# Kernel tuning notes

Hardware: AMD Instinct MI355X
Metric: run time of the kernel (lower is better)

Reference implementation:

```python
import jax, jax.numpy as jnp
import numpy as np

LATENT_DIM = 64
K = 128


def setup_inputs() -> dict:
    key = jax.random.key(0)
    ks = jax.random.split(key, 7)
    B, T, N, d, k = 64, 1024, 1024, LATENT_DIM, K
    return {
        "review_seq": jax.random.normal(ks[0], (B, T, d), dtype=jnp.float32),
        "post_seq": jax.random.normal(ks[1], (B, N, d), dtype=jnp.float32),
        "Wl": jax.random.normal(ks[2], (d, d), dtype=jnp.float32) * 0.05,
        "Wr": jax.random.normal(ks[3], (k, d), dtype=jnp.float32) * 0.05,
        "Wp": jax.random.normal(ks[4], (k, d), dtype=jnp.float32) * 0.05,
        "whr": jax.random.normal(ks[5], (1, k), dtype=jnp.float32) * 0.05,
        "whp": jax.random.normal(ks[6], (1, k), dtype=jnp.float32) * 0.05,
    }


def reference(review_seq, post_seq, Wl, Wr, Wp, whr, whp):
    # L[b,t,n] = tanh(review @ Wl @ post^T)
    L = jnp.tanh(jnp.einsum('btd,dD,bnD->btn', review_seq, Wl, post_seq))
    # Hp[b,k,n] = tanh(Wp @ post^T + Wr @ review^T @ L)
    Hp = jnp.tanh(jnp.einsum('kd,bnd->bkn', Wp, post_seq)
                  + jnp.einsum('kd,btd,btn->bkn', Wr, review_seq, L))
    # Hr[b,k,t] = tanh(Wr @ review^T + Wp @ post^T @ L^T)
    Hr = jnp.tanh(jnp.einsum('kd,btd->bkt', Wr, review_seq)
                  + jnp.einsum('kd,bnd,btn->bkt', Wp, post_seq, L))
    # attention weights over post (n) and review (t) positions
    Ap = jax.nn.softmax(jnp.einsum('yk,bkn->bn', whp, Hp), axis=-1)
    Ar = jax.nn.softmax(jnp.einsum('yk,bkt->bt', whr, Hr), axis=-1)
    co_p = jnp.einsum('bnd,bn->bd', post_seq, Ap)
    co_r = jnp.einsum('btd,bt->bd', review_seq, Ar)
    return jnp.concatenate([co_p, co_r], axis=1)  # [B, 2*latent_dim]
```

## Files before the change

### kernel.cpp

```cpp
#include <hip/hip_runtime.h>
#include <hip/hip_bf16.h>


typedef __attribute__((ext_vector_type(8))) short bfrag;
typedef __attribute__((ext_vector_type(4))) float ffrag;

typedef const __attribute__((address_space(1))) unsigned GAS_U;
typedef __attribute__((address_space(3))) unsigned LAS_U;

__device__ __forceinline__ void gload16(const void* g, void* l) {
  __builtin_amdgcn_global_load_lds((GAS_U*)g, (LAS_U*)l, 16, 0, 0);
}

__device__ __forceinline__ unsigned short f2b(float f) {
  unsigned u = __builtin_bit_cast(unsigned, f);
  u += 0x7FFFu + ((u >> 16) & 1u);
  return (unsigned short)(u >> 16);
}
__device__ __forceinline__ float b2f(unsigned short h) {
  return __builtin_bit_cast(float, (unsigned)h << 16);
}
__device__ __forceinline__ float ftanh(float x) {
  float e = __builtin_amdgcn_exp2f(x * 2.88539008177792681f);
  return fmaf(-2.0f, __builtin_amdgcn_rcpf(e + 1.0f), 1.0f);
}
__device__ __forceinline__ unsigned cvtpk(float lo, float hi) {
  unsigned r;
  asm("v_cvt_pk_bf16_f32 %0, %1, %2" : "=v"(r) : "v"(lo), "v"(hi));
  return r;
}

#define MFMA(a, b, c) __builtin_amdgcn_mfma_f32_16x16x32_bf16((a), (b), (c), 0, 0, 0)

__global__ __launch_bounds__(256) void prep_kernel(
    const float* __restrict__ review, const float* __restrict__ post,
    const float* __restrict__ Wl, const float* __restrict__ Wr,
    const float* __restrict__ Wp,
    unsigned short* __restrict__ RWb, unsigned short* __restrict__ Rb,
    unsigned short* __restrict__ Pb, unsigned short* __restrict__ postb)
{
  const int chunk = blockIdx.x, b = blockIdx.y, side = blockIdx.z;
  const int tid = threadIdx.x, lane = tid & 63, w = tid >> 6;
  const int lr = lane & 15, lg = lane >> 4;
  const int r0 = chunk * 128;

  __shared__ __align__(16) unsigned short seqs[128][72];
  __shared__ __align__(16) unsigned short wgt[128][72];
  __shared__ __align__(16) unsigned short wlt[64][72];

  const float* seq = (side == 0) ? review : post;
#pragma unroll
  for (int jj = 0; jj < 8; ++jj) {
    int e = tid + jj * 256;
    int r = e >> 4, d4 = (e & 15) * 4;
    float4 v = *(const float4*)(seq + ((size_t)(b * 1024 + r0 + r)) * 64 + d4);
    unsigned lo = ((unsigned)f2b(v.y) << 16) | f2b(v.x);
    unsigned hi = ((unsigned)f2b(v.w) << 16) | f2b(v.z);
    *(uint2*)&seqs[r][d4] = make_uint2(lo, hi);
    if (side == 1)
      *(uint2*)(postb + ((size_t)(b * 1024 + r0 + r)) * 64 + d4) = make_uint2(lo, hi);
  }
  const float* wkd = (side == 0) ? Wr : Wp;
#pragma unroll
  for (int jj = 0; jj < 8; ++jj) {
    int e = tid + jj * 256;
    int k = e >> 4, d4 = (e & 15) * 4;
    float4 v = *(const float4*)(wkd + k * 64 + d4);
    unsigned lo = ((unsigned)f2b(v.y) << 16) | f2b(v.x);
    unsigned hi = ((unsigned)f2b(v.w) << 16) | f2b(v.z);
    *(uint2*)&wgt[k][d4] = make_uint2(lo, hi);
  }
  if (side == 0) {
    for (int i = tid; i < 64 * 64; i += 256) {
      int d = i >> 6, c = i & 63;
      wlt[c][d] = f2b(Wl[d * 64 + c]);
    }
  }
  __syncthreads();

  if (side == 0) {
    ffrag acc[2][4] = {};
#pragma unroll
    for (int ks = 0; ks < 2; ++ks)
#pragma unroll
      for (int ts = 0; ts < 2; ++ts) {
        bfrag a = *(const bfrag*)&seqs[w * 32 + ts * 16 + lr][ks * 32 + lg * 8];
#pragma unroll
        for (int is = 0; is < 4; ++is) {
          bfrag bb = *(const bfrag*)&wlt[is * 16 + lr][ks * 32 + lg * 8];
          acc[ts][is] = MFMA(a, bb, acc[ts][is]);
        }
      }
#pragma unroll
    for (int ts = 0; ts < 2; ++ts)
#pragma unroll
      for (int is = 0; is < 4; ++is)
#pragma unroll
        for (int j = 0; j < 4; ++j) {
          int t = r0 + w * 32 + ts * 16 + lg * 4 + j;
          int i2 = is * 16 + lr;
          RWb[((size_t)(b * 1024 + t)) * 64 + i2] = f2b(acc[ts][is][j]);
        }
  }
  {
    ffrag acc[2][8] = {};
#pragma unroll
    for (int ks = 0; ks < 2; ++ks)
#pragma unroll
      for (int ksb = 0; ksb < 2; ++ksb) {
        bfrag a = *(const bfrag*)&wgt[w * 32 + ksb * 16 + lr][ks * 32 + lg * 8];
#pragma unroll
        for (int ts = 0; ts < 8; ++ts) {
          bfrag bb = *(const bfrag*)&seqs[ts * 16 + lr][ks * 32 + lg * 8];
          acc[ksb][ts] = MFMA(a, bb, acc[ksb][ts]);
        }
      }
    unsigned short* dst = (side == 0) ? Rb : Pb;
#pragma unroll
    for (int ksb = 0; ksb < 2; ++ksb)
#pragma unroll
      for (int ts = 0; ts < 8; ++ts)
#pragma unroll
        for (int j = 0; j < 4; ++j) {
          int k = w * 32 + ksb * 16 + lg * 4 + j;
          int t = r0 + ts * 16 + lr;
          dst[((size_t)(b * 128 + k)) * 1024 + t] = f2b(acc[ksb][ts][j]);
        }
  }
}

__global__ __launch_bounds__(256, 4) void hz_kernel(
    const unsigned short* __restrict__ RWb, const unsigned short* __restrict__ Rb,
    const unsigned short* __restrict__ Pb, const unsigned short* __restrict__ postb,
    const float* __restrict__ whp, const float* __restrict__ whr,
    float* __restrict__ zp, float* __restrict__ zr)
{
  const int orig = blockIdx.x;
  const int swz = (orig & 7) * 128 + (orig >> 3);
  const int strip = swz & 7, pair = swz >> 3;
  const int b = pair & 63, role = pair >> 6;
  const int s0 = strip * 128;
  const int tid = threadIdx.x, lane = tid & 63, w = tid >> 6;
  const int lr = lane & 15, lg = lane >> 4;

  const unsigned short* resident = role ? RWb : postb;
  const unsigned short* chunkseq = role ? postb : RWb;
  const unsigned short* coeff    = role ? Pb : Rb;
  const unsigned short* addterm  = role ? Rb : Pb;
  const float* wh                = role ? whr : whp;
  float* zout                    = role ? zr : zp;

  __shared__ __align__(16) char smem[32768];
  float* zacc = (float*)(smem + 24576);

  const int crow = (w << 3) + (lane >> 3), cslot = lane & 7;
  const char* csrc = (const char*)chunkseq + (size_t)b * 131072
                     + crow * 128 + ((cslot ^ (crow & 7)) << 4);
  const int kk = ((w & 1) << 6) + lane;
  const char* ksrc = (const char*)coeff + (size_t)b * 262144
                     + (size_t)kk * 2048 + (w >> 1) * 16;
  const int woff = w << 10;

  bfrag bb[2][2];
  {
    const char* rbase = (const char*)resident + ((size_t)(b * 1024 + s0)) * 128;
#pragma unroll
    for (int ks = 0; ks < 2; ++ks)
#pragma unroll
      for (int ns = 0; ns < 2; ++ns)
        bb[ks][ns] = *(const bfrag*)(rbase + (w * 32 + ns * 16 + lr) * 128 + ks * 64 + lg * 16);
  }

  gload16(csrc, smem + woff);
  gload16(ksrc, smem + 8192 + woff);
  gload16(ksrc + 32, smem + 12288 + woff);
  __syncthreads();

  ffrag acc[2][8] = {};
  int cur = 0;

#pragma unroll 2
  for (int tc = 0; tc < 32; ++tc) {
    if (tc < 31) {
      const int nb = cur ^ 1;
      const char* cs = csrc + (size_t)(tc + 1) * 4096;
      const char* ks2 = ksrc + (tc + 1) * 64;
      gload16(cs, smem + nb * 4096 + woff);
      gload16(ks2, smem + 8192 + nb * 8192 + woff);
      gload16(ks2 + 32, smem + 8192 + nb * 8192 + 4096 + woff);
    }

    {
      const char* rwc = smem + cur * 4096;
#pragma unroll
      for (int ts = 0; ts < 2; ++ts) {
        ffrag la[2] = {};
#pragma unroll
        for (int ks = 0; ks < 2; ++ks) {
          const int arow = ts * 16 + lr;
          bfrag a = *(const bfrag*)(rwc + arow * 128 + (((ks * 4 + lg) ^ (arow & 7)) << 4));
#pragma unroll
          for (int ns = 0; ns < 2; ++ns)
            la[ns] = MFMA(a, bb[ks][ns], la[ns]);
        }
#pragma unroll
        for (int ns = 0; ns < 2; ++ns) {
          const int res = w * 32 + ns * 16 + lr;
          uint2 pkv;
          pkv.x = cvtpk(ftanh(la[ns][0]), ftanh(la[ns][1]));
          pkv.y = cvtpk(ftanh(la[ns][2]), ftanh(la[ns][3]));
          *(uint2*)(smem + 24576 + (ts * 2 + (lg >> 1)) * 2048 + res * 16 + (lg & 1) * 8) = pkv;
        }
      }
    }
    __syncthreads();

    {
      const char* rlc = smem + 8192 + cur * 8192;
      bfrag a0 = *(const bfrag*)(rlc + lg * 2048 + (w * 32 + lr) * 16);
      bfrag a1 = *(const bfrag*)(rlc + lg * 2048 + (w * 32 + 16 + lr) * 16);
#pragma unroll
      for (int ns = 0; ns < 8; ++ns) {
        bfrag bbr = *(const bfrag*)(smem + 24576 + lg * 2048 + (ns * 16 + lr) * 16);
        acc[0][ns] = MFMA(a0, bbr, acc[0][ns]);
        acc[1][ns] = MFMA(a1, bbr, acc[1][ns]);
      }
    }
    __syncthreads();
    cur ^= 1;
  }

  float zpart[8] = {0, 0, 0, 0, 0, 0, 0, 0};
#pragma unroll
  for (int ksb = 0; ksb < 2; ++ksb)
#pragma unroll
    for (int j = 0; j < 4; ++j) {
      const int k = w * 32 + ksb * 16 + lg * 4 + j;
      const float whk = wh[k];
      const unsigned short* arow = addterm + ((size_t)(b * 128 + k)) * 1024 + s0;
#pragma unroll
      for (int ns = 0; ns < 8; ++ns) {
        const int res = ns * 16 + lr;
        float h = ftanh(acc[ksb][ns][j] + b2f(arow[res]));
        zpart[ns] += whk * h;
      }
    }
#pragma unroll
  for (int ns = 0; ns < 8; ++ns) {
    zpart[ns] += __shfl_xor(zpart[ns], 16);
    zpart[ns] += __shfl_xor(zpart[ns], 32);
  }
  if (lg == 0) {
#pragma unroll
    for (int ns = 0; ns < 8; ++ns) zacc[w * 128 + ns * 16 + lr] = zpart[ns];
  }
  __syncthreads();
  if (tid < 128)
    zout[(size_t)b * 1024 + s0 + tid] =
        zacc[tid] + zacc[128 + tid] + zacc[256 + tid] + zacc[384 + tid];
}

__global__ __launch_bounds__(1024) void final_kernel(
    const float* __restrict__ review, const float* __restrict__ post,
    const float* __restrict__ zp, const float* __restrict__ zr,
    float* __restrict__ out)
{
  const int b = blockIdx.x, side = blockIdx.y, tid = threadIdx.x;
  const int wid = tid >> 6, lane = tid & 63;
  __shared__ float zl[1024];
  __shared__ float red[16];
  __shared__ float cacc[16][64];

  const float* z = (side == 0) ? zp : zr;
  const float* seq = (side == 0) ? post : review;

  float v = z[(size_t)b * 1024 + tid];
  zl[tid] = v;
  float m = v;
#pragma unroll
  for (int off = 32; off; off >>= 1) m = fmaxf(m, __shfl_xor(m, off));
  if (lane == 0) red[wid] = m;
  __syncthreads();
  m = red[0];
#pragma unroll
  for (int i = 1; i < 16; ++i) m = fmaxf(m, red[i]);
  __syncthreads();

  float e = __expf(v - m);
  zl[tid] = e;
  float sm = e;
#pragma unroll
  for (int off = 32; off; off >>= 1) sm += __shfl_xor(sm, off);
  if (lane == 0) red[wid] = sm;
  __syncthreads();
  sm = red[0];
#pragma unroll
  for (int i = 1; i < 16; ++i) sm += red[i];
  const float inv = 1.0f / sm;

  const int d = lane;
  float a = 0.f;
  for (int n = wid * 64; n < wid * 64 + 64; ++n)
    a += zl[n] * seq[((size_t)(b * 1024 + n)) * 64 + d];
  cacc[wid][d] = a;
  __syncthreads();
  if (tid < 64) {
    float s = 0.f;
#pragma unroll
    for (int g = 0; g < 16; ++g) s += cacc[g][tid];
    out[b * 128 + side * 64 + tid] = s * inv;
  }
}

extern "C" void kernel_launch(void* const* d_in, const int* in_sizes, int n_in,
                              void* d_out, int out_size, void* d_ws, size_t ws_size,
                              hipStream_t stream) {
  const float* review = (const float*)d_in[0];
  const float* post   = (const float*)d_in[1];
  const float* Wl     = (const float*)d_in[2];
  const float* Wr     = (const float*)d_in[3];
  const float* Wp     = (const float*)d_in[4];
  const float* whr    = (const float*)d_in[5];
  const float* whp    = (const float*)d_in[6];
  float* out = (float*)d_out;

  char* ws = (char*)d_ws;
  unsigned short* RWb   = (unsigned short*)(ws);
  unsigned short* Rb    = (unsigned short*)(ws + (size_t)8  * 1048576);
  unsigned short* Pb    = (unsigned short*)(ws + (size_t)24 * 1048576);
  unsigned short* postb = (unsigned short*)(ws + (size_t)40 * 1048576);
  float* zp = (float*)(ws + (size_t)48 * 1048576);
  float* zr = (float*)(ws + (size_t)48 * 1048576 + 262144);

  prep_kernel<<<dim3(8, 64, 2), dim3(256), 0, stream>>>(
      review, post, Wl, Wr, Wp, RWb, Rb, Pb, postb);
  hz_kernel<<<dim3(1024), dim3(256), 0, stream>>>(
      RWb, Rb, Pb, postb, whp, whr, zp, zr);
  final_kernel<<<dim3(64, 2), dim3(1024), 0, stream>>>(
      review, post, zp, zr, out);
}
```

Before: 103.7 us.

## Keep tanh(L) tile in registers as MFMA operand, retile coefficient layout

The second GEMM in hz_kernel now takes the tanh'd L tile straight from registers. It feeds the packed bf16 values as operands to a 16x16x16 MFMA instead of writing them to shared memory and reading them back. That removes the LDS round trip and one __syncthreads per iteration. To support this, prep_kernel writes Rb/Pb in a tiled layout that matches the new fragment loads, and the epilogue reduces with lane shuffles instead of through shared memory. The cost is using the smaller-K MFMA instruction (more instructions per FLOP) and an inline-asm accumulator constraint.

```diff
diff --git a/kernel.cpp b/kernel.cpp
--- a/kernel.cpp
+++ b/kernel.cpp
@@ -3,6 +3,7 @@
 
 
 typedef __attribute__((ext_vector_type(8))) short bfrag;
+typedef __attribute__((ext_vector_type(4))) short bfrag4;
 typedef __attribute__((ext_vector_type(4))) float ffrag;
 
 typedef const __attribute__((address_space(1))) unsigned GAS_U;
@@ -31,6 +32,11 @@
 }
 
 #define MFMA(a, b, c) __builtin_amdgcn_mfma_f32_16x16x32_bf16((a), (b), (c), 0, 0, 0)
+
+__device__ __forceinline__ void mfma16(bfrag4 a, bfrag4 b, ffrag& c) {
+  asm volatile("v_mfma_f32_16x16x16_bf16 %0, %1, %2, %0" : "+a"(c) : "v"(a), "v"(b));
+}
+
 
 __global__ __launch_bounds__(256) void prep_kernel(
     const float* __restrict__ review, const float* __restrict__ post,
@@ -115,17 +121,18 @@
           acc[ksb][ts] = MFMA(a, bb, acc[ksb][ts]);
         }
       }
-    unsigned short* dst = (side == 0) ? Rb : Pb;
+    char* dstb = (char*)((side == 0) ? Rb : Pb) + (size_t)b * 262144
+                 + (size_t)chunk * 4 * 8192;
 #pragma unroll
     for (int ksb = 0; ksb < 2; ++ksb)
 #pragma unroll
-      for (int ts = 0; ts < 8; ++ts)
-#pragma unroll
-        for (int j = 0; j < 4; ++j) {
-          int k = w * 32 + ksb * 16 + lg * 4 + j;
-          int t = r0 + ts * 16 + lr;
-          dst[((size_t)(b * 128 + k)) * 1024 + t] = f2b(acc[ksb][ts][j]);
-        }
+      for (int ts2 = 0; ts2 < 8; ++ts2) {
+        char* base = dstb + (ts2 >> 1) * 8192 + (ts2 & 1) * 4096
+                     + (w * 2 + ksb) * 512 + (lr >> 2) * 128 + (lr & 3) * 2;
+#pragma unroll
+        for (int j = 0; j < 4; ++j)
+          *(unsigned short*)(base + (lg * 4 + j) * 8) = f2b(acc[ksb][ts2][j]);
+      }
   }
 }
 
@@ -150,16 +157,13 @@
   const float* wh                = role ? whr : whp;
   float* zout                    = role ? zr : zp;
 
-  __shared__ __align__(16) char smem[32768];
-  float* zacc = (float*)(smem + 24576);
-
-  const int crow = (w << 3) + (lane >> 3), cslot = lane & 7;
+  __shared__ __align__(16) char smem[24576];
+  const int woff = w << 10;
+
+  const int crow = tid >> 3, cslot = tid & 7;
   const char* csrc = (const char*)chunkseq + (size_t)b * 131072
                      + crow * 128 + ((cslot ^ (crow & 7)) << 4);
-  const int kk = ((w & 1) << 6) + lane;
-  const char* ksrc = (const char*)coeff + (size_t)b * 262144
-                     + (size_t)kk * 2048 + (w >> 1) * 16;
-  const int woff = w << 10;
+  const char* ksrc = (const char*)coeff + (size_t)b * 262144 + tid * 16;
 
   bfrag bb[2][2];
   {
@@ -167,97 +171,89 @@
 #pragma unroll
     for (int ks = 0; ks < 2; ++ks)
 #pragma unroll
-      for (int ns = 0; ns < 2; ++ns)
-        bb[ks][ns] = *(const bfrag*)(rbase + (w * 32 + ns * 16 + lr) * 128 + ks * 64 + lg * 16);
+      for (int rs = 0; rs < 2; ++rs)
+        bb[ks][rs] = *(const bfrag*)(rbase + (w * 32 + rs * 16 + lr) * 128 + ks * 64 + lg * 16);
   }
 
   gload16(csrc, smem + woff);
   gload16(ksrc, smem + 8192 + woff);
-  gload16(ksrc + 32, smem + 12288 + woff);
+  gload16(ksrc + 4096, smem + 8192 + 4096 + woff);
   __syncthreads();
 
   ffrag acc[2][8] = {};
-  int cur = 0;
 
 #pragma unroll 2
   for (int tc = 0; tc < 32; ++tc) {
+    const int cur = tc & 1;
     if (tc < 31) {
       const int nb = cur ^ 1;
-      const char* cs = csrc + (size_t)(tc + 1) * 4096;
-      const char* ks2 = ksrc + (tc + 1) * 64;
-      gload16(cs, smem + nb * 4096 + woff);
-      gload16(ks2, smem + 8192 + nb * 8192 + woff);
-      gload16(ks2 + 32, smem + 8192 + nb * 8192 + 4096 + woff);
-    }
-
-    {
-      const char* rwc = smem + cur * 4096;
+      gload16(csrc + (size_t)(tc + 1) * 4096, smem + nb * 4096 + woff);
+      gload16(ksrc + (size_t)(tc + 1) * 8192, smem + 8192 + nb * 8192 + woff);
+      gload16(ksrc + (size_t)(tc + 1) * 8192 + 4096, smem + 8192 + nb * 8192 + 4096 + woff);
+    }
+
+    const char* rwc = smem + cur * 4096;
+    uint2 pk[2][2];
+#pragma unroll
+    for (int ts = 0; ts < 2; ++ts) {
+      ffrag la[2] = {};
+#pragma unroll
+      for (int ks = 0; ks < 2; ++ks) {
+        const int arow = ts * 16 + lr;
+        bfrag a = *(const bfrag*)(rwc + arow * 128 + (((ks * 4 + lg) ^ (arow & 7)) << 4));
+        la[0] = MFMA(a, bb[ks][0], la[0]);
+        la[1] = MFMA(a, bb[ks][1], la[1]);
+      }
+#pragma unroll
+      for (int rs = 0; rs < 2; ++rs) {
+        pk[ts][rs].x = cvtpk(ftanh(la[rs][0]), ftanh(la[rs][1]));
+        pk[ts][rs].y = cvtpk(ftanh(la[rs][2]), ftanh(la[rs][3]));
+      }
+    }
+
+    const char* rlc = smem + 8192 + cur * 8192;
+#pragma unroll
+    for (int kt = 0; kt < 8; ++kt) {
 #pragma unroll
       for (int ts = 0; ts < 2; ++ts) {
-        ffrag la[2] = {};
-#pragma unroll
-        for (int ks = 0; ks < 2; ++ks) {
-          const int arow = ts * 16 + lr;
-          bfrag a = *(const bfrag*)(rwc + arow * 128 + (((ks * 4 + lg) ^ (arow & 7)) << 4));
-#pragma unroll
-          for (int ns = 0; ns < 2; ++ns)
-            la[ns] = MFMA(a, bb[ks][ns], la[ns]);
-        }
-#pragma unroll
-        for (int ns = 0; ns < 2; ++ns) {
-          const int res = w * 32 + ns * 16 + lr;
-          uint2 pkv;
-          pkv.x = cvtpk(ftanh(la[ns][0]), ftanh(la[ns][1]));
-          pkv.y = cvtpk(ftanh(la[ns][2]), ftanh(la[ns][3]));
-          *(uint2*)(smem + 24576 + (ts * 2 + (lg >> 1)) * 2048 + res * 16 + (lg & 1) * 8) = pkv;
-        }
+        bfrag4 bk = *(const bfrag4*)(rlc + ts * 4096 + kt * 512 + lg * 128 + lr * 8);
+        mfma16(__builtin_bit_cast(bfrag4, pk[ts][0]), bk, acc[0][kt]);
+        mfma16(__builtin_bit_cast(bfrag4, pk[ts][1]), bk, acc[1][kt]);
       }
     }
     __syncthreads();
-
-    {
-      const char* rlc = smem + 8192 + cur * 8192;
-      bfrag a0 = *(const bfrag*)(rlc + lg * 2048 + (w * 32 + lr) * 16);
-      bfrag a1 = *(const bfrag*)(rlc + lg * 2048 + (w * 32 + 16 + lr) * 16);
-#pragma unroll
-      for (int ns = 0; ns < 8; ++ns) {
-        bfrag bbr = *(const bfrag*)(smem + 24576 + lg * 2048 + (ns * 16 + lr) * 16);
-        acc[0][ns] = MFMA(a0, bbr, acc[0][ns]);
-        acc[1][ns] = MFMA(a1, bbr, acc[1][ns]);
-      }
-    }
-    __syncthreads();
-    cur ^= 1;
-  }
-
-  float zpart[8] = {0, 0, 0, 0, 0, 0, 0, 0};
-#pragma unroll
-  for (int ksb = 0; ksb < 2; ++ksb)
+  }
+
+  float whs[8];
+#pragma unroll
+  for (int kt = 0; kt < 8; ++kt) whs[kt] = wh[kt * 16 + lr];
+
+  const char* abase = (const char*)addterm + (size_t)b * 262144
+                      + (size_t)(strip * 4 + w) * 8192 + lg * 128 + lr * 8;
+  float zsum[2][4] = {};
+#pragma unroll
+  for (int rs = 0; rs < 2; ++rs)
+#pragma unroll
+    for (int kt = 0; kt < 8; ++kt) {
+      uint2 av = *(const uint2*)(abase + rs * 4096 + kt * 512);
+      const float whk = whs[kt];
+      zsum[rs][0] += whk * ftanh(acc[rs][kt][0] + b2f((unsigned short)(av.x & 0xFFFF)));
+      zsum[rs][1] += whk * ftanh(acc[rs][kt][1] + b2f((unsigned short)(av.x >> 16)));
+      zsum[rs][2] += whk * ftanh(acc[rs][kt][2] + b2f((unsigned short)(av.y & 0xFFFF)));
+      zsum[rs][3] += whk * ftanh(acc[rs][kt][3] + b2f((unsigned short)(av.y >> 16)));
+    }
+#pragma unroll
+  for (int rs = 0; rs < 2; ++rs)
 #pragma unroll
     for (int j = 0; j < 4; ++j) {
-      const int k = w * 32 + ksb * 16 + lg * 4 + j;
-      const float whk = wh[k];
-      const unsigned short* arow = addterm + ((size_t)(b * 128 + k)) * 1024 + s0;
-#pragma unroll
-      for (int ns = 0; ns < 8; ++ns) {
-        const int res = ns * 16 + lr;
-        float h = ftanh(acc[ksb][ns][j] + b2f(arow[res]));
-        zpart[ns] += whk * h;
-      }
-    }
-#pragma unroll
-  for (int ns = 0; ns < 8; ++ns) {
-    zpart[ns] += __shfl_xor(zpart[ns], 16);
-    zpart[ns] += __shfl_xor(zpart[ns], 32);
-  }
-  if (lg == 0) {
-#pragma unroll
-    for (int ns = 0; ns < 8; ++ns) zacc[w * 128 + ns * 16 + lr] = zpart[ns];
-  }
-  __syncthreads();
-  if (tid < 128)
-    zout[(size_t)b * 1024 + s0 + tid] =
-        zacc[tid] + zacc[128 + tid] + zacc[256 + tid] + zacc[384 + tid];
+      float v = zsum[rs][j];
+      v += __shfl_xor(v, 1);
+      v += __shfl_xor(v, 2);
+      v += __shfl_xor(v, 4);
+      v += __shfl_xor(v, 8);
+      if (lr == 0)
+        zout[(size_t)b * 1024 + s0 + w * 32 + rs * 16 + lg * 4 + j] = v;
+    }
 }
 
 __global__ __launch_bounds__(1024) void final_kernel(
```

Result: slower. 184.7 us (+78.0%).

## Split hz_kernel into 64-wide strips with 8 waves per block

Applied to the files above, without the earlier changes.

The hz kernel now handles 64 resident positions per block instead of 128 and runs 8 waves of 512 threads, with a grid of 2048 blocks. Each wave computes one 16x16 L tile and a 16x64 slice of the second GEMM, so per-thread accumulator registers drop from 32 to 16 floats. Only half the waves load the chunk sequence, and the loop is no longer unrolled. The aim is higher occupancy and more parallelism, at the cost of reloading the streamed chunk and coefficient data twice as often overall and doing more cross-wave reduction.

```diff
diff --git a/kernel.cpp b/kernel.cpp
--- a/kernel.cpp
+++ b/kernel.cpp
@@ -129,17 +129,17 @@
   }
 }
 
-__global__ __launch_bounds__(256, 4) void hz_kernel(
+__global__ __launch_bounds__(512, 6) void hz_kernel(
     const unsigned short* __restrict__ RWb, const unsigned short* __restrict__ Rb,
     const unsigned short* __restrict__ Pb, const unsigned short* __restrict__ postb,
     const float* __restrict__ whp, const float* __restrict__ whr,
     float* __restrict__ zp, float* __restrict__ zr)
 {
   const int orig = blockIdx.x;
-  const int swz = (orig & 7) * 128 + (orig >> 3);
-  const int strip = swz & 7, pair = swz >> 3;
+  const int swz = (orig & 7) * 256 + (orig >> 3);
+  const int strip = swz & 15, pair = swz >> 4;
   const int b = pair & 63, role = pair >> 6;
-  const int s0 = strip * 128;
+  const int s0 = strip * 64;
   const int tid = threadIdx.x, lane = tid & 63, w = tid >> 6;
   const int lr = lane & 15, lg = lane >> 4;
 
@@ -150,7 +150,8 @@
   const float* wh                = role ? whr : whp;
   float* zout                    = role ? zr : zp;
 
-  __shared__ __align__(16) char smem[32768];
+  __shared__ __align__(16) char smem[28672];
+  char* ll = smem + 24576;
   float* zacc = (float*)(smem + 24576);
 
   const int crow = (w << 3) + (lane >> 3), cslot = lane & 7;
@@ -161,103 +162,86 @@
                      + (size_t)kk * 2048 + (w >> 1) * 16;
   const int woff = w << 10;
 
-  bfrag bb[2][2];
+  const int ts = w >> 2, rs = w & 3;
+  bfrag rb[2];
   {
     const char* rbase = (const char*)resident + ((size_t)(b * 1024 + s0)) * 128;
 #pragma unroll
     for (int ks = 0; ks < 2; ++ks)
-#pragma unroll
-      for (int ns = 0; ns < 2; ++ns)
-        bb[ks][ns] = *(const bfrag*)(rbase + (w * 32 + ns * 16 + lr) * 128 + ks * 64 + lg * 16);
-  }
-
-  gload16(csrc, smem + woff);
+      rb[ks] = *(const bfrag*)(rbase + (rs * 16 + lr) * 128 + ks * 64 + lg * 16);
+  }
+
+  if (w < 4) gload16(csrc, smem + woff);
   gload16(ksrc, smem + 8192 + woff);
-  gload16(ksrc + 32, smem + 12288 + woff);
-  __syncthreads();
-
-  ffrag acc[2][8] = {};
-  int cur = 0;
-
-#pragma unroll 2
+  __syncthreads();
+
+  ffrag acc[4] = {};
+
+#pragma unroll 1
   for (int tc = 0; tc < 32; ++tc) {
+    const int cur = tc & 1, nb = cur ^ 1;
     if (tc < 31) {
-      const int nb = cur ^ 1;
-      const char* cs = csrc + (size_t)(tc + 1) * 4096;
-      const char* ks2 = ksrc + (tc + 1) * 64;
-      gload16(cs, smem + nb * 4096 + woff);
-      gload16(ks2, smem + 8192 + nb * 8192 + woff);
-      gload16(ks2 + 32, smem + 8192 + nb * 8192 + 4096 + woff);
+      if (w < 4) gload16(csrc + (size_t)(tc + 1) * 4096, smem + nb * 4096 + woff);
+      gload16(ksrc + (size_t)(tc + 1) * 64, smem + 8192 + nb * 8192 + woff);
     }
 
     {
       const char* rwc = smem + cur * 4096;
-#pragma unroll
-      for (int ts = 0; ts < 2; ++ts) {
-        ffrag la[2] = {};
-#pragma unroll
-        for (int ks = 0; ks < 2; ++ks) {
-          const int arow = ts * 16 + lr;
-          bfrag a = *(const bfrag*)(rwc + arow * 128 + (((ks * 4 + lg) ^ (arow & 7)) << 4));
-#pragma unroll
-          for (int ns = 0; ns < 2; ++ns)
-            la[ns] = MFMA(a, bb[ks][ns], la[ns]);
-        }
-#pragma unroll
-        for (int ns = 0; ns < 2; ++ns) {
-          const int res = w * 32 + ns * 16 + lr;
-          uint2 pkv;
-          pkv.x = cvtpk(ftanh(la[ns][0]), ftanh(la[ns][1]));
-          pkv.y = cvtpk(ftanh(la[ns][2]), ftanh(la[ns][3]));
-          *(uint2*)(smem + 24576 + (ts * 2 + (lg >> 1)) * 2048 + res * 16 + (lg & 1) * 8) = pkv;
-        }
+      const int arow = ts * 16 + lr;
+      ffrag la = {};
+#pragma unroll
+      for (int ks = 0; ks < 2; ++ks) {
+        bfrag a = *(const bfrag*)(rwc + arow * 128 + (((ks * 4 + lg) ^ (arow & 7)) << 4));
+        la = MFMA(a, rb[ks], la);
       }
+      uint2 pk;
+      pk.x = cvtpk(ftanh(la[0]), ftanh(la[1]));
+      pk.y = cvtpk(ftanh(la[2]), ftanh(la[3]));
+      *(uint2*)(ll + (ts * 2 + (lg >> 1)) * 1024 + (rs * 16 + lr) * 16 + (lg & 1) * 8) = pk;
     }
     __syncthreads();
 
     {
       const char* rlc = smem + 8192 + cur * 8192;
-      bfrag a0 = *(const bfrag*)(rlc + lg * 2048 + (w * 32 + lr) * 16);
-      bfrag a1 = *(const bfrag*)(rlc + lg * 2048 + (w * 32 + 16 + lr) * 16);
-#pragma unroll
-      for (int ns = 0; ns < 8; ++ns) {
-        bfrag bbr = *(const bfrag*)(smem + 24576 + lg * 2048 + (ns * 16 + lr) * 16);
-        acc[0][ns] = MFMA(a0, bbr, acc[0][ns]);
-        acc[1][ns] = MFMA(a1, bbr, acc[1][ns]);
+      bfrag a0 = *(const bfrag*)(rlc + lg * 2048 + (w * 16 + lr) * 16);
+#pragma unroll
+      for (int nt = 0; nt < 4; ++nt) {
+        bfrag bbr = *(const bfrag*)(ll + lg * 1024 + (nt * 16 + lr) * 16);
+        acc[nt] = MFMA(a0, bbr, acc[nt]);
       }
     }
     __syncthreads();
-    cur ^= 1;
-  }
-
-  float zpart[8] = {0, 0, 0, 0, 0, 0, 0, 0};
-#pragma unroll
-  for (int ksb = 0; ksb < 2; ++ksb)
-#pragma unroll
-    for (int j = 0; j < 4; ++j) {
-      const int k = w * 32 + ksb * 16 + lg * 4 + j;
-      const float whk = wh[k];
-      const unsigned short* arow = addterm + ((size_t)(b * 128 + k)) * 1024 + s0;
-#pragma unroll
-      for (int ns = 0; ns < 8; ++ns) {
-        const int res = ns * 16 + lr;
-        float h = ftanh(acc[ksb][ns][j] + b2f(arow[res]));
-        zpart[ns] += whk * h;
-      }
-    }
-#pragma unroll
-  for (int ns = 0; ns < 8; ++ns) {
-    zpart[ns] += __shfl_xor(zpart[ns], 16);
-    zpart[ns] += __shfl_xor(zpart[ns], 32);
+  }
+
+  const float4 whs4 = *(const float4*)(wh + w * 16 + lg * 4);
+  float zpart[4] = {0, 0, 0, 0};
+#pragma unroll
+  for (int j = 0; j < 4; ++j) {
+    const int k = w * 16 + lg * 4 + j;
+    const float whk = ((const float*)&whs4)[j];
+    const unsigned short* arow = addterm + ((size_t)(b * 128 + k)) * 1024 + s0;
+#pragma unroll
+    for (int nt = 0; nt < 4; ++nt) {
+      const int res = nt * 16 + lr;
+      zpart[nt] += whk * ftanh(acc[nt][j] + b2f(arow[res]));
+    }
+  }
+#pragma unroll
+  for (int nt = 0; nt < 4; ++nt) {
+    zpart[nt] += __shfl_xor(zpart[nt], 16);
+    zpart[nt] += __shfl_xor(zpart[nt], 32);
   }
   if (lg == 0) {
 #pragma unroll
-    for (int ns = 0; ns < 8; ++ns) zacc[w * 128 + ns * 16 + lr] = zpart[ns];
-  }
-  __syncthreads();
-  if (tid < 128)
-    zout[(size_t)b * 1024 + s0 + tid] =
-        zacc[tid] + zacc[128 + tid] + zacc[256 + tid] + zacc[384 + tid];
+    for (int nt = 0; nt < 4; ++nt) zacc[w * 64 + nt * 16 + lr] = zpart[nt];
+  }
+  __syncthreads();
+  if (tid < 64) {
+    float s = 0.f;
+#pragma unroll
+    for (int g = 0; g < 8; ++g) s += zacc[g * 64 + tid];
+    zout[(size_t)b * 1024 + s0 + tid] = s;
+  }
 }
 
 __global__ __launch_bounds__(1024) void final_kernel(
@@ -334,7 +318,7 @@
 
   prep_kernel<<<dim3(8, 64, 2), dim3(256), 0, stream>>>(
       review, post, Wl, Wr, Wp, RWb, Rb, Pb, postb);
-  hz_kernel<<<dim3(1024), dim3(256), 0, stream>>>(
+  hz_kernel<<<dim3(2048), dim3(512), 0, stream>>>(
       RWb, Rb, Pb, postb, whp, whr, zp, zr);
   final_kernel<<<dim3(64, 2), dim3(1024), 0, stream>>>(
       review, post, zp, zr, out);
```

Measured after the change: 122.0 us. +17.6%, slower.
